# Kernel optimization log

Measured on AMD Instinct MI355X. Metric: run time of the kernel, lower is better.

Reference implementation:

```python
import jax, jax.numpy as jnp
import numpy as np

N, E = 50000, 800000          # nodes, edges
DIN, HEAD, HD = 128, 4, 16    # input dim, heads, per-head dim
DOUT = HEAD * HD              # 64 = head*hd
NEG_SLOPE = 0.01              # torch LeakyReLU default


def _lin(key, fan_in, fan_out):
    # torch nn.Linear default init: U(-1/sqrt(fan_in), 1/sqrt(fan_in))
    kw, kb = jax.random.split(key)
    s = 1.0 / np.sqrt(fan_in)
    W = jax.random.uniform(kw, (fan_in, fan_out), jnp.float32, -s, s)
    b = jax.random.uniform(kb, (fan_out,), jnp.float32, -s, s)
    return W, b


def setup_inputs() -> dict:
    key = jax.random.key(0)
    ks = jax.random.split(key, 8)
    x = jax.random.normal(ks[0], (N, DIN), jnp.float32)
    src = jax.random.randint(ks[1], (E,), 0, N, jnp.int32)
    dst = jax.random.randint(ks[2], (E,), 0, N, jnp.int32)
    Ws, bs = _lin(ks[3], DIN, DOUT)   # relation_aware src linear
    Wd, bd = _lin(ks[4], DIN, DOUT)   # relation_aware dst linear
    Wl, bl = _lin(ks[5], DIN, DOUT)   # w_liner
    Wa, ba = _lin(ks[6], 3 * HD, 1)   # atten
    return dict(x=x, src=src, dst=dst, Ws=Ws, bs=bs, Wd=Wd, bd=bd,
                Wl=Wl, bl=bl, Wa=Wa, ba=ba)


def reference(x, src, dst, Ws, bs, Wd, bd, Wl, bl, Wa, ba):
    # sign_edges: relation-aware per-edge feature edge_sum  [E, DOUT]
    er = jnp.tanh(x[src] @ Ws + bs + (x[dst] @ Wd + bd))

    # w_liner on node features  [N, DOUT]
    h = x @ Wl + bl

    # message: per-edge, per-head concat + linear + leakyrelu score
    sf = h[src].reshape(E, HEAD, HD)
    df = h[dst].reshape(E, HEAD, HD)
    ef = er.reshape(E, HEAD, HD)
    z = jnp.concatenate([sf, df, ef], axis=-1)        # [E, HEAD, 3*HD]
    a = z @ Wa + ba                                    # [E, HEAD, 1]
    a = jnp.where(a >= 0, a, NEG_SLOPE * a)            # leaky relu

    # reduce: mailbox softmax over incoming edges of each dst node
    m = jax.ops.segment_max(a, dst, num_segments=N)    # [N, HEAD, 1]
    m = jnp.where(jnp.isfinite(m), m, 0.0)             # empty mailboxes -> 0
    e = jnp.exp(a - m[dst])
    s = jax.ops.segment_sum(e, dst, num_segments=N)    # [N, HEAD, 1]
    attn = e / jnp.maximum(s[dst], 1e-38)

    out = jax.ops.segment_sum(attn * sf, dst, num_segments=N)
    out = out.reshape(N, DOUT)                         # [N, head*hd]

    # edge_s: mean of edge_sum over incoming edges per node
    deg = jax.ops.segment_sum(jnp.ones((E, 1), x.dtype), dst, num_segments=N)
    edge_s = jax.ops.segment_sum(er, dst, num_segments=N) / jnp.maximum(deg, 1.0)

    return (edge_s, out, h)  # if_sum=False branch: h already [N, head*hd]
```

## Files before the change

kernel.cpp:

```cpp
#include <hip/hip_runtime.h>
#include <math.h>

#define DIN   128
#define DOUT  64
#define NHEAD 4
#define HD    16

typedef __attribute__((ext_vector_type(8))) short bf16x8;
typedef __attribute__((ext_vector_type(8))) unsigned short u16x8;
typedef __attribute__((ext_vector_type(4))) float f32x4;

__device__ __forceinline__ unsigned short f2bf(float f) {
    union { float f; unsigned u; } v; v.f = f;
    unsigned r = v.u + 0x7FFF + ((v.u >> 16) & 1);
    return (unsigned short)(r >> 16);
}
__device__ __forceinline__ float bf2f(unsigned short s) {
    union { unsigned u; float f; } v; v.u = ((unsigned)s) << 16; return v.f;
}

__global__ __launch_bounds__(256)
void k_init(const float* __restrict__ Ws, const float* __restrict__ Wd,
            const float* __restrict__ Wl, short* __restrict__ wT,
            int* __restrict__ degi, int* __restrict__ counter, int N) {
    const int bid = blockIdx.x, tid = threadIdx.x;
    if (bid < 96) {
        const int idx = bid * 256 + tid;
        const int n = idx >> 7, k = idx & 127;
        float v;
        if (n < 64)       v = Ws[k * DOUT + n];
        else if (n < 128) v = Wd[k * DOUT + (n - 64)];
        else              v = Wl[k * DOUT + (n - 128)];
        wT[idx] = (short)f2bf(v);
        if (bid == 0 && tid == 0) *counter = 0;
        return;
    }
    const int i = (bid - 96) * 256 + tid;
    if (i < N) degi[i] = 0;
}

__global__ __launch_bounds__(256)
void k_proj_hist(const float* __restrict__ x, const short* __restrict__ wT,
                 const float* __restrict__ bs, const float* __restrict__ bd,
                 const float* __restrict__ bl, const float* __restrict__ Wa,
                 unsigned short* __restrict__ packed_bf,
                 float* __restrict__ xd, float* __restrict__ alpha_s,
                 float* __restrict__ alpha_d, float* __restrict__ h_out, int N,
                 const int* __restrict__ dst, int* __restrict__ degi,
                 int* __restrict__ rank, int E, int NPJ, int NHB) {
    __shared__ short xs[64 * 136];
    const int bid = blockIdx.x, tid = threadIdx.x;

    if (bid & 1) {
        const int hi = bid >> 1;
        if (hi >= NHB) return;
        const int e0 = (hi * 256 + tid) * 4;
        if (e0 + 3 < E) {
            const int4 d = *(const int4*)&dst[e0];
            int4 r;
            r.x = atomicAdd(&degi[d.x], 1);
            r.y = atomicAdd(&degi[d.y], 1);
            r.z = atomicAdd(&degi[d.z], 1);
            r.w = atomicAdd(&degi[d.w], 1);
            *(int4*)&rank[e0] = r;
        } else {
            for (int e = e0; e < E; ++e) rank[e] = atomicAdd(&degi[dst[e]], 1);
        }
        return;
    }

    const int pj = bid >> 1;
    if (pj >= NPJ) return;
    const int wave = tid >> 6, lane = tid & 63;
    const int lam = lane & 15, g = lane >> 4;
    const int n0 = pj * 64;

    {
        const int r = tid >> 2, c0 = (tid & 3) * 32;
        const int nn = n0 + r;
#pragma unroll
        for (int j = 0; j < 8; ++j) {
            float4 v = make_float4(0.f, 0.f, 0.f, 0.f);
            if (nn < N) v = ((const float4*)x)[(size_t)nn * 32 + (c0 >> 2) + j];
            short4 h4;
            h4.x = (short)f2bf(v.x); h4.y = (short)f2bf(v.y);
            h4.z = (short)f2bf(v.z); h4.w = (short)f2bf(v.w);
            *(short4*)&xs[r * 136 + c0 + j * 4] = h4;
        }
    }
    __syncthreads();

    bf16x8 afr[4];
#pragma unroll
    for (int ks = 0; ks < 4; ++ks)
        afr[ks] = *(const bf16x8*)&xs[(wave * 16 + lam) * 136 + ks * 32 + g * 8];

    f32x4 acc[12];
#pragma unroll
    for (int c = 0; c < 12; ++c) acc[c] = (f32x4){0.f, 0.f, 0.f, 0.f};

#pragma unroll
    for (int c = 0; c < 12; ++c) {
#pragma unroll
        for (int ks = 0; ks < 4; ++ks) {
            const bf16x8 b = *(const bf16x8*)&wT[(c * 16 + lam) * 128 + ks * 32 + g * 8];
            acc[c] = __builtin_amdgcn_mfma_f32_16x16x32_bf16(afr[ks], b, acc[c], 0, 0, 0);
        }
    }

    float bsv[4], bdv[4], blv[4];
#pragma unroll
    for (int c = 0; c < 4; ++c) {
        bsv[c] = bs[c * 16 + lam];
        bdv[c] = bd[c * 16 + lam];
        blv[c] = bl[c * 16 + lam];
    }
    const float waS = Wa[lam], waD = Wa[16 + lam];
    const int cc_base = (lam >> 2), t_sl = lam & 3;

#pragma unroll
    for (int i = 0; i < 4; ++i) {
        const int node = n0 + wave * 16 + g * 4 + i;
        float xsv[4], xdv[4], hv[4];
#pragma unroll
        for (int c = 0; c < 4; ++c) {
            xsv[c] = acc[c][i]     + bsv[c];
            xdv[c] = acc[4 + c][i] + bdv[c];
            hv[c]  = acc[8 + c][i] + blv[c];
        }
        float p0 = hv[0] * waS, p1 = hv[1] * waS, p2 = hv[2] * waS, p3 = hv[3] * waS;
        float q0 = hv[0] * waD, q1 = hv[1] * waD, q2 = hv[2] * waD, q3 = hv[3] * waD;
#pragma unroll
        for (int off = 1; off < 16; off <<= 1) {
            p0 += __shfl_xor(p0, off); p1 += __shfl_xor(p1, off);
            p2 += __shfl_xor(p2, off); p3 += __shfl_xor(p3, off);
            q0 += __shfl_xor(q0, off); q1 += __shfl_xor(q1, off);
            q2 += __shfl_xor(q2, off); q3 += __shfl_xor(q3, off);
        }
        if (node < N) {
            const size_t rowb = (size_t)node * 128;
#pragma unroll
            for (int c = 0; c < 4; ++c) {
                const int cc = c * 4 + cc_base;
                packed_bf[rowb + cc * 8 + t_sl]     = f2bf(xsv[c]);
                packed_bf[rowb + cc * 8 + 4 + t_sl] = f2bf(hv[c]);
                xd   [(size_t)node * DOUT + c * 16 + lam] = xdv[c];
                h_out[(size_t)node * DOUT + c * 16 + lam] = hv[c];
            }
            if (lam == 0) {
                *(f32x4*)&alpha_s[(size_t)node * NHEAD] = (f32x4){p0, p1, p2, p3};
                *(f32x4*)&alpha_d[(size_t)node * NHEAD] = (f32x4){q0, q1, q2, q3};
            }
        }
    }
}

__global__ __launch_bounds__(1024)
void k_scan(const int* __restrict__ degi, int* __restrict__ excl,
            int* __restrict__ bsum, int* __restrict__ boff,
            int* __restrict__ total, int* __restrict__ counter, int N, int NB) {
    __shared__ int wsum[16];
    __shared__ int amLast;
    const int tid = threadIdx.x, lane = tid & 63, wid = tid >> 6;
    const int i = blockIdx.x * 1024 + tid;
    int v = (i < N) ? degi[i] : 0;
    int incl = v;
#pragma unroll
    for (int off = 1; off < 64; off <<= 1) {
        int t = __shfl_up(incl, off);
        if (lane >= off) incl += t;
    }
    if (lane == 63) wsum[wid] = incl;
    __syncthreads();
    if (tid < 16) {
        int t = wsum[tid];
#pragma unroll
        for (int off = 1; off < 16; off <<= 1) {
            int u = __shfl_up(t, off);
            if (tid >= off) t += u;
        }
        wsum[tid] = t;
    }
    __syncthreads();
    const int base = (wid > 0) ? wsum[wid - 1] : 0;
    if (i < N) excl[i] = incl - v + base;
    if (tid == 1023) atomicExch(&bsum[blockIdx.x], wsum[15]);
    __syncthreads();
    if (tid == 0) {
        __threadfence();
        amLast = (atomicAdd(counter, 1) == NB - 1) ? 1 : 0;
    }
    __syncthreads();
    if (amLast && tid < 64) {
        int b = (tid < NB) ? atomicAdd(&bsum[tid], 0) : 0;
        int inc = b;
#pragma unroll
        for (int off = 1; off < 64; off <<= 1) {
            int t = __shfl_up(inc, off);
            if (lane >= off) inc += t;
        }
        if (tid < NB) boff[tid] = inc - b;
        if (tid == 63) *total = inc;
    }
}

__global__ __launch_bounds__(256)
void k_scatter(const int* __restrict__ src, const int* __restrict__ dst,
               const int* __restrict__ rp_raw, const int* __restrict__ boff,
               const int* __restrict__ rank, int* __restrict__ srcs_sorted, int E) {
    const int e0 = (blockIdx.x * 256 + threadIdx.x) * 4;
    if (e0 + 3 < E) {
        const int4 s = *(const int4*)&src[e0];
        const int4 d = *(const int4*)&dst[e0];
        const int4 r = *(const int4*)&rank[e0];
        srcs_sorted[rp_raw[d.x] + boff[d.x >> 10] + r.x] = s.x;
        srcs_sorted[rp_raw[d.y] + boff[d.y >> 10] + r.y] = s.y;
        srcs_sorted[rp_raw[d.z] + boff[d.z >> 10] + r.z] = s.z;
        srcs_sorted[rp_raw[d.w] + boff[d.w >> 10] + r.w] = s.w;
    } else {
        for (int e = e0; e < E; ++e) {
            const int d = dst[e];
            srcs_sorted[rp_raw[d] + boff[d >> 10] + rank[e]] = src[e];
        }
    }
}

__global__ __launch_bounds__(256, 8)
void k_aggregate(const int* __restrict__ rp_raw, const int* __restrict__ boff,
                 const int* __restrict__ total, const int* __restrict__ srcs,
                 const unsigned short* __restrict__ packed_bf,
                 const float* __restrict__ xd,
                 const float* __restrict__ alpha_s, const float* __restrict__ alpha_d,
                 const float* __restrict__ Wa, const float* __restrict__ ba,
                 float* __restrict__ edge_s, float* __restrict__ out, int N) {
    const int lane = threadIdx.x & 63;
    const int n = blockIdx.x * 4 + (threadIdx.x >> 6);
    if (n >= N) return;
    const int g = lane >> 4, lam = lane & 15;
    const int hd = lam >> 2, q = lam & 3;

    const int start = rp_raw[n] + boff[n >> 10];
    const int end = (n + 1 < N) ? (rp_raw[n + 1] + boff[(n + 1) >> 10]) : *total;
    const int deg = end - start;
    const int last = end - 1;

    const float4 xd4 = *(const float4*)&xd[(size_t)n * DOUT + lam * 4];
    const float4 wa4 = *(const float4*)&Wa[32 + q * 4];
    const float adb  = alpha_d[n * NHEAD + hd] + ba[0];

    float es0=0.f,es1=0.f,es2=0.f,es3=0.f;
    float o0=0.f,o1=0.f,o2=0.f,o3=0.f;
    float s = 0.f;

    const int niter = (deg + 3) >> 2;
    int e = start + g;

    float vm0=0.f, vm1=0.f, vm2=0.f;
    u16x8 pk0=(u16x8){0,0,0,0,0,0,0,0}, pk1=pk0, pk2=pk0;
    float as0=0.f, as1=0.f, as2=0.f;
    if (niter > 0) {
        {
            vm0 = (e < end) ? 1.f : 0.f;
            const int sn = srcs[min(e, last)];
            pk0 = *(const u16x8*)&packed_bf[(size_t)sn * 128 + lam * 8];
            as0 = alpha_s[sn * NHEAD + hd];
        }
        {
            const int e1 = e + 4;
            vm1 = (e1 < end) ? 1.f : 0.f;
            const int sn = srcs[min(e1, last)];
            pk1 = *(const u16x8*)&packed_bf[(size_t)sn * 128 + lam * 8];
            as1 = alpha_s[sn * NHEAD + hd];
        }
        {
            const int e2 = e + 8;
            vm2 = (e2 < end) ? 1.f : 0.f;
            const int sn = srcs[min(e2, last)];
            pk2 = *(const u16x8*)&packed_bf[(size_t)sn * 128 + lam * 8];
            as2 = alpha_s[sn * NHEAD + hd];
        }
    }

    for (int it = 0; it < niter; ++it) {
        float vmn = 0.f, asn = 0.f;
        u16x8 pkn = (u16x8){0,0,0,0,0,0,0,0};
        const int e3 = e + 12;
        if (it + 3 < niter) {
            vmn = (e3 < end) ? 1.f : 0.f;
            const int sn = srcs[min(e3, last)];
            pkn = *(const u16x8*)&packed_bf[(size_t)sn * 128 + lam * 8];
            asn = alpha_s[sn * NHEAD + hd];
        }

        const float t0 = __expf(2.f * (bf2f(pk0[0]) + xd4.x));
        const float t1 = __expf(2.f * (bf2f(pk0[1]) + xd4.y));
        const float t2 = __expf(2.f * (bf2f(pk0[2]) + xd4.z));
        const float t3 = __expf(2.f * (bf2f(pk0[3]) + xd4.w));
        const float er0 = fmaf(-2.f, __builtin_amdgcn_rcpf(t0 + 1.f), 1.f);
        const float er1 = fmaf(-2.f, __builtin_amdgcn_rcpf(t1 + 1.f), 1.f);
        const float er2 = fmaf(-2.f, __builtin_amdgcn_rcpf(t2 + 1.f), 1.f);
        const float er3 = fmaf(-2.f, __builtin_amdgcn_rcpf(t3 + 1.f), 1.f);
        es0 = fmaf(er0, vm0, es0); es1 = fmaf(er1, vm0, es1);
        es2 = fmaf(er2, vm0, es2); es3 = fmaf(er3, vm0, es3);

        float p = er0 * wa4.x;
        p = fmaf(er1, wa4.y, p);
        p = fmaf(er2, wa4.z, p);
        p = fmaf(er3, wa4.w, p);
        p += __shfl_xor(p, 1);
        p += __shfl_xor(p, 2);

        float a = as0 + adb + p;
        a = (a >= 0.f) ? a : 0.01f * a;
        const float w = __expf(a) * vm0;
        s += w;
        o0 = fmaf(w, bf2f(pk0[4]), o0); o1 = fmaf(w, bf2f(pk0[5]), o1);
        o2 = fmaf(w, bf2f(pk0[6]), o2); o3 = fmaf(w, bf2f(pk0[7]), o3);

        vm0 = vm1; pk0 = pk1; as0 = as1;
        vm1 = vm2; pk1 = pk2; as1 = as2;
        vm2 = vmn; pk2 = pkn; as2 = asn;
        e += 4;
    }

#pragma unroll
    for (int off = 16; off < 64; off <<= 1) {
        es0 += __shfl_xor(es0, off); es1 += __shfl_xor(es1, off);
        es2 += __shfl_xor(es2, off); es3 += __shfl_xor(es3, off);
        o0  += __shfl_xor(o0,  off); o1  += __shfl_xor(o1,  off);
        o2  += __shfl_xor(o2,  off); o3  += __shfl_xor(o3,  off);
        s   += __shfl_xor(s,   off);
    }

    if (g == 0) {
        const float inv_s = __builtin_amdgcn_rcpf(fmaxf(s, 1e-38f));
        const float inv_d = __builtin_amdgcn_rcpf(fmaxf((float)deg, 1.0f));
        const size_t od = (size_t)n * DOUT + lam * 4;
        *(f32x4*)&out[od]    = (f32x4){o0 * inv_s, o1 * inv_s, o2 * inv_s, o3 * inv_s};
        *(f32x4*)&edge_s[od] = (f32x4){es0 * inv_d, es1 * inv_d, es2 * inv_d, es3 * inv_d};
    }
}

extern "C" void kernel_launch(void* const* d_in, const int* in_sizes, int n_in,
                              void* d_out, int out_size, void* d_ws, size_t ws_size,
                              hipStream_t stream) {
    const float* x  = (const float*)d_in[0];
    const int*   src= (const int*)  d_in[1];
    const int*   dst= (const int*)  d_in[2];
    const float* Ws = (const float*)d_in[3];
    const float* bs = (const float*)d_in[4];
    const float* Wd = (const float*)d_in[5];
    const float* bd = (const float*)d_in[6];
    const float* Wl = (const float*)d_in[7];
    const float* bl = (const float*)d_in[8];
    const float* Wa = (const float*)d_in[9];
    const float* ba = (const float*)d_in[10];

    const int N = in_sizes[0] / DIN;
    const int E = in_sizes[1];
    const int NB = (N + 1023) / 1024;

    float* out_f = (float*)d_out;
    float* edge_s_out = out_f;
    float* out_attn   = out_f + (size_t)N * DOUT;
    float* h_out      = out_f + 2 * (size_t)N * DOUT;

    char* ws = (char*)d_ws;
    size_t o = 0;
    unsigned short* packed_bf = (unsigned short*)(ws + o); o += (size_t)N * 128 * 2;
    float* xd      = (float*)(ws + o); o += (size_t)N * DOUT * 4;
    float* alpha_s = (float*)(ws + o); o += (size_t)N * NHEAD * 4;
    float* alpha_d = (float*)(ws + o); o += (size_t)N * NHEAD * 4;
    int*   degi    = (int*)  (ws + o); o += (size_t)N * 4;
    int*   counter = (int*)  (ws + o); o += 64;
    int*   rp_raw  = (int*)  (ws + o); o += (size_t)(N + 1) * 4;
    int*   rank    = (int*)  (ws + o); o += (size_t)E * 4;
    int*   srcs    = (int*)  (ws + o); o += (size_t)E * 4;
    int*   bsum    = (int*)  (ws + o); o += 64 * 4;
    int*   boff    = (int*)  (ws + o); o += 64 * 4;
    int*   total   = (int*)  (ws + o); o += 64;
    short* wT      = (short*)(ws + o); o += (size_t)192 * 128 * 2;

    k_init<<<96 + (N + 255) / 256, 256, 0, stream>>>(Ws, Wd, Wl, wT, degi, counter, N);

    const int NPJ = (N + 63) / 64;
    const int NHB = (E + 1023) / 1024;
    const int GC  = 2 * ((NPJ > NHB) ? NPJ : NHB);
    k_proj_hist<<<GC, 256, 0, stream>>>(x, wT, bs, bd, bl, Wa,
                                        packed_bf, xd, alpha_s, alpha_d, h_out, N,
                                        dst, degi, rank, E, NPJ, NHB);

    k_scan<<<NB, 1024, 0, stream>>>(degi, rp_raw, bsum, boff, total, counter, N, NB);

    k_scatter<<<((E + 3) / 4 + 255) / 256, 256, 0, stream>>>(src, dst, rp_raw, boff,
                                                             rank, srcs, E);

    k_aggregate<<<(N + 3) / 4, 256, 0, stream>>>(rp_raw, boff, total, srcs,
                                                 packed_bf, xd,
                                                 alpha_s, alpha_d, Wa, ba,
                                                 edge_s_out, out_attn, N);
}
```

Baseline: 130.9 us.

## Replace per-node atomic CSR build with two-level bucket sort by destination

Replaces the per-edge global atomic degree histogram, multi-block scan and scattered rank-based placement with a bucketed counting sort. Edges are first binned into 128-node buckets using shared-memory histograms, then sorted within each bucket in shared memory to produce row_ptr and sorted sources. This removes high-contention global atomics and random scattered writes, at the cost of an extra pass, an intermediate (src,dst) pair buffer and one extra kernel launch. Within-bucket order becomes nondeterministic, so the summation order in aggregation can change.

After: 136.6 us. +4.4%, slower.

```diff
diff --git a/kernel.cpp b/kernel.cpp
--- a/kernel.cpp
+++ b/kernel.cpp
@@ -5,6 +5,8 @@
 #define DOUT  64
 #define NHEAD 4
 #define HD    16
+#define BKT_SH 7
+#define BKT_SZ 128
 
 typedef __attribute__((ext_vector_type(8))) short bf16x8;
 typedef __attribute__((ext_vector_type(8))) unsigned short u16x8;
@@ -22,7 +24,7 @@
 __global__ __launch_bounds__(256)
 void k_init(const float* __restrict__ Ws, const float* __restrict__ Wd,
             const float* __restrict__ Wl, short* __restrict__ wT,
-            int* __restrict__ degi, int* __restrict__ counter, int N) {
+            int* __restrict__ bucket_cnt, int NBK) {
     const int bid = blockIdx.x, tid = threadIdx.x;
     if (bid < 96) {
         const int idx = bid * 256 + tid;
@@ -32,40 +34,47 @@
         else if (n < 128) v = Wd[k * DOUT + (n - 64)];
         else              v = Wl[k * DOUT + (n - 128)];
         wT[idx] = (short)f2bf(v);
-        if (bid == 0 && tid == 0) *counter = 0;
         return;
     }
     const int i = (bid - 96) * 256 + tid;
-    if (i < N) degi[i] = 0;
+    if (i <= NBK) bucket_cnt[i] = 0;
 }
 
 __global__ __launch_bounds__(256)
-void k_proj_hist(const float* __restrict__ x, const short* __restrict__ wT,
-                 const float* __restrict__ bs, const float* __restrict__ bd,
-                 const float* __restrict__ bl, const float* __restrict__ Wa,
-                 unsigned short* __restrict__ packed_bf,
-                 float* __restrict__ xd, float* __restrict__ alpha_s,
-                 float* __restrict__ alpha_d, float* __restrict__ h_out, int N,
-                 const int* __restrict__ dst, int* __restrict__ degi,
-                 int* __restrict__ rank, int E, int NPJ, int NHB) {
+void k_proj_cnt(const float* __restrict__ x, const short* __restrict__ wT,
+                const float* __restrict__ bs, const float* __restrict__ bd,
+                const float* __restrict__ bl, const float* __restrict__ Wa,
+                unsigned short* __restrict__ packed_bf,
+                float* __restrict__ xd, float* __restrict__ alpha_s,
+                float* __restrict__ alpha_d, float* __restrict__ h_out, int N,
+                const int* __restrict__ dst, int* __restrict__ bucket_cnt,
+                int E, int NPJ, int NCB, int NBK) {
     __shared__ short xs[64 * 136];
+    __shared__ int  lhist[392];
     const int bid = blockIdx.x, tid = threadIdx.x;
 
     if (bid & 1) {
-        const int hi = bid >> 1;
-        if (hi >= NHB) return;
-        const int e0 = (hi * 256 + tid) * 4;
-        if (e0 + 3 < E) {
-            const int4 d = *(const int4*)&dst[e0];
-            int4 r;
-            r.x = atomicAdd(&degi[d.x], 1);
-            r.y = atomicAdd(&degi[d.y], 1);
-            r.z = atomicAdd(&degi[d.z], 1);
-            r.w = atomicAdd(&degi[d.w], 1);
-            *(int4*)&rank[e0] = r;
-        } else {
-            for (int e = e0; e < E; ++e) rank[e] = atomicAdd(&degi[dst[e]], 1);
-        }
+        const int ci = bid >> 1;
+        if (ci >= NCB) return;
+        for (int i = tid; i < NBK; i += 256) lhist[i] = 0;
+        __syncthreads();
+        const int base0 = ci * 4096;
+#pragma unroll
+        for (int k = 0; k < 4; ++k) {
+            const int e0 = base0 + k * 1024 + tid * 4;
+            if (e0 + 3 < E) {
+                const int4 d = *(const int4*)&dst[e0];
+                atomicAdd(&lhist[d.x >> BKT_SH], 1);
+                atomicAdd(&lhist[d.y >> BKT_SH], 1);
+                atomicAdd(&lhist[d.z >> BKT_SH], 1);
+                atomicAdd(&lhist[d.w >> BKT_SH], 1);
+            } else {
+                for (int e = e0; e < E; ++e) atomicAdd(&lhist[dst[e] >> BKT_SH], 1);
+            }
+        }
+        __syncthreads();
+        for (int i = tid; i < NBK; i += 256)
+            if (lhist[i]) atomicAdd(&bucket_cnt[i], lhist[i]);
         return;
     }
 
@@ -155,15 +164,13 @@
     }
 }
 
-__global__ __launch_bounds__(1024)
-void k_scan(const int* __restrict__ degi, int* __restrict__ excl,
-            int* __restrict__ bsum, int* __restrict__ boff,
-            int* __restrict__ total, int* __restrict__ counter, int N, int NB) {
-    __shared__ int wsum[16];
-    __shared__ int amLast;
+__global__ __launch_bounds__(512)
+void k_scan_buckets(const int* __restrict__ bucket_cnt,
+                    int* __restrict__ bucket_base, int* __restrict__ bucket_cursor,
+                    int NBK) {
+    __shared__ int wsum[8];
     const int tid = threadIdx.x, lane = tid & 63, wid = tid >> 6;
-    const int i = blockIdx.x * 1024 + tid;
-    int v = (i < N) ? degi[i] : 0;
+    int v = (tid < NBK) ? bucket_cnt[tid] : 0;
     int incl = v;
 #pragma unroll
     for (int off = 1; off < 64; off <<= 1) {
@@ -172,10 +179,10 @@
     }
     if (lane == 63) wsum[wid] = incl;
     __syncthreads();
-    if (tid < 16) {
+    if (tid < 8) {
         int t = wsum[tid];
 #pragma unroll
-        for (int off = 1; off < 16; off <<= 1) {
+        for (int off = 1; off < 8; off <<= 1) {
             int u = __shfl_up(t, off);
             if (tid >= off) t += u;
         }
@@ -183,51 +190,110 @@
     }
     __syncthreads();
     const int base = (wid > 0) ? wsum[wid - 1] : 0;
-    if (i < N) excl[i] = incl - v + base;
-    if (tid == 1023) atomicExch(&bsum[blockIdx.x], wsum[15]);
-    __syncthreads();
-    if (tid == 0) {
-        __threadfence();
-        amLast = (atomicAdd(counter, 1) == NB - 1) ? 1 : 0;
-    }
-    __syncthreads();
-    if (amLast && tid < 64) {
-        int b = (tid < NB) ? atomicAdd(&bsum[tid], 0) : 0;
-        int inc = b;
+    const int excl = incl - v + base;
+    if (tid < NBK) {
+        bucket_base[tid]   = excl;
+        bucket_cursor[tid] = excl;
+    }
+    if (tid == 0) bucket_base[NBK] = wsum[7];
+}
+
+__global__ __launch_bounds__(256)
+void k_bucket_scatter(const int* __restrict__ src, const int* __restrict__ dst,
+                      int* __restrict__ bucket_cursor, int2* __restrict__ pairs,
+                      int E, int NBK) {
+    __shared__ int lhist[392];
+    __shared__ int lcur[392];
+    const int tid = threadIdx.x;
+    const int base0 = blockIdx.x * 4096;
+    for (int i = tid; i < NBK; i += 256) lhist[i] = 0;
+    __syncthreads();
+#pragma unroll
+    for (int k = 0; k < 4; ++k) {
+        const int e0 = base0 + k * 1024 + tid * 4;
+        if (e0 + 3 < E) {
+            const int4 d = *(const int4*)&dst[e0];
+            atomicAdd(&lhist[d.x >> BKT_SH], 1);
+            atomicAdd(&lhist[d.y >> BKT_SH], 1);
+            atomicAdd(&lhist[d.z >> BKT_SH], 1);
+            atomicAdd(&lhist[d.w >> BKT_SH], 1);
+        } else {
+            for (int e = e0; e < E; ++e) atomicAdd(&lhist[dst[e] >> BKT_SH], 1);
+        }
+    }
+    __syncthreads();
+    for (int i = tid; i < NBK; i += 256)
+        lcur[i] = lhist[i] ? atomicAdd(&bucket_cursor[i], lhist[i]) : 0;
+    __syncthreads();
+#pragma unroll
+    for (int k = 0; k < 4; ++k) {
+        const int e0 = base0 + k * 1024 + tid * 4;
+        if (e0 + 3 < E) {
+            const int4 s = *(const int4*)&src[e0];
+            const int4 d = *(const int4*)&dst[e0];
+            int p;
+            p = atomicAdd(&lcur[d.x >> BKT_SH], 1); pairs[p] = make_int2(s.x, d.x);
+            p = atomicAdd(&lcur[d.y >> BKT_SH], 1); pairs[p] = make_int2(s.y, d.y);
+            p = atomicAdd(&lcur[d.z >> BKT_SH], 1); pairs[p] = make_int2(s.z, d.z);
+            p = atomicAdd(&lcur[d.w >> BKT_SH], 1); pairs[p] = make_int2(s.w, d.w);
+        } else {
+            for (int e = e0; e < E; ++e) {
+                const int d = dst[e];
+                const int p = atomicAdd(&lcur[d >> BKT_SH], 1);
+                pairs[p] = make_int2(src[e], d);
+            }
+        }
+    }
+}
+
+__global__ __launch_bounds__(256)
+void k_bucket_rank(const int2* __restrict__ pairs, const int* __restrict__ bucket_base,
+                   int* __restrict__ row_ptr, int* __restrict__ srcs,
+                   int N, int NBK) {
+    __shared__ int hist[BKT_SZ];
+    __shared__ int cursor[BKT_SZ];
+    __shared__ int wtot[2];
+    const int b = blockIdx.x, tid = threadIdx.x;
+    const int n0 = b << BKT_SH;
+    const int ebase = bucket_base[b];
+    const int ecnt  = bucket_base[b + 1] - ebase;
+
+    if (tid < BKT_SZ) hist[tid] = 0;
+    __syncthreads();
+    for (int i = tid; i < ecnt; i += 256)
+        atomicAdd(&hist[pairs[ebase + i].y & (BKT_SZ - 1)], 1);
+    __syncthreads();
+
+    int v = 0, incl = 0;
+    const int lane = tid & 63, wid = tid >> 6;
+    if (tid < BKT_SZ) {
+        v = hist[tid];
+        incl = v;
 #pragma unroll
         for (int off = 1; off < 64; off <<= 1) {
-            int t = __shfl_up(inc, off);
-            if (lane >= off) inc += t;
-        }
-        if (tid < NB) boff[tid] = inc - b;
-        if (tid == 63) *total = inc;
-    }
-}
-
-__global__ __launch_bounds__(256)
-void k_scatter(const int* __restrict__ src, const int* __restrict__ dst,
-               const int* __restrict__ rp_raw, const int* __restrict__ boff,
-               const int* __restrict__ rank, int* __restrict__ srcs_sorted, int E) {
-    const int e0 = (blockIdx.x * 256 + threadIdx.x) * 4;
-    if (e0 + 3 < E) {
-        const int4 s = *(const int4*)&src[e0];
-        const int4 d = *(const int4*)&dst[e0];
-        const int4 r = *(const int4*)&rank[e0];
-        srcs_sorted[rp_raw[d.x] + boff[d.x >> 10] + r.x] = s.x;
-        srcs_sorted[rp_raw[d.y] + boff[d.y >> 10] + r.y] = s.y;
-        srcs_sorted[rp_raw[d.z] + boff[d.z >> 10] + r.z] = s.z;
-        srcs_sorted[rp_raw[d.w] + boff[d.w >> 10] + r.w] = s.w;
-    } else {
-        for (int e = e0; e < E; ++e) {
-            const int d = dst[e];
-            srcs_sorted[rp_raw[d] + boff[d >> 10] + rank[e]] = src[e];
-        }
+            int t = __shfl_up(incl, off);
+            if (lane >= off) incl += t;
+        }
+        if (lane == 63) wtot[wid] = incl;
+    }
+    __syncthreads();
+    if (tid < BKT_SZ) {
+        const int excl = incl - v + ((wid == 1) ? wtot[0] : 0);
+        if (n0 + tid < N) row_ptr[n0 + tid] = ebase + excl;
+        cursor[tid] = excl;
+    }
+    if (b == NBK - 1 && tid == 0) row_ptr[N] = bucket_base[NBK];
+    __syncthreads();
+
+    for (int i = tid; i < ecnt; i += 256) {
+        const int2 pr = pairs[ebase + i];
+        const int slot = atomicAdd(&cursor[pr.y & (BKT_SZ - 1)], 1);
+        srcs[ebase + slot] = pr.x;
     }
 }
 
 __global__ __launch_bounds__(256, 8)
-void k_aggregate(const int* __restrict__ rp_raw, const int* __restrict__ boff,
-                 const int* __restrict__ total, const int* __restrict__ srcs,
+void k_aggregate(const int* __restrict__ row_ptr, const int* __restrict__ srcs,
                  const unsigned short* __restrict__ packed_bf,
                  const float* __restrict__ xd,
                  const float* __restrict__ alpha_s, const float* __restrict__ alpha_d,
@@ -239,8 +305,8 @@
     const int g = lane >> 4, lam = lane & 15;
     const int hd = lam >> 2, q = lam & 3;
 
-    const int start = rp_raw[n] + boff[n >> 10];
-    const int end = (n + 1 < N) ? (rp_raw[n + 1] + boff[(n + 1) >> 10]) : *total;
+    const int start = row_ptr[n];
+    const int end   = row_ptr[n + 1];
     const int deg = end - start;
     const int last = end - 1;
 
@@ -358,7 +424,7 @@
 
     const int N = in_sizes[0] / DIN;
     const int E = in_sizes[1];
-    const int NB = (N + 1023) / 1024;
+    const int NBK = (N + BKT_SZ - 1) >> BKT_SH;
 
     float* out_f = (float*)d_out;
     float* edge_s_out = out_f;
@@ -371,32 +437,30 @@
     float* xd      = (float*)(ws + o); o += (size_t)N * DOUT * 4;
     float* alpha_s = (float*)(ws + o); o += (size_t)N * NHEAD * 4;
     float* alpha_d = (float*)(ws + o); o += (size_t)N * NHEAD * 4;
-    int*   degi    = (int*)  (ws + o); o += (size_t)N * 4;
-    int*   counter = (int*)  (ws + o); o += 64;
-    int*   rp_raw  = (int*)  (ws + o); o += (size_t)(N + 1) * 4;
-    int*   rank    = (int*)  (ws + o); o += (size_t)E * 4;
+    int*   row_ptr = (int*)  (ws + o); o += (size_t)(N + 1) * 4;
     int*   srcs    = (int*)  (ws + o); o += (size_t)E * 4;
-    int*   bsum    = (int*)  (ws + o); o += 64 * 4;
-    int*   boff    = (int*)  (ws + o); o += 64 * 4;
-    int*   total   = (int*)  (ws + o); o += 64;
+    int2*  pairs   = (int2*) (ws + o); o += (size_t)E * 8;
+    int*   bucket_cnt    = (int*)(ws + o); o += 512 * 4;
+    int*   bucket_base   = (int*)(ws + o); o += 513 * 4;
+    int*   bucket_cursor = (int*)(ws + o); o += 512 * 4;
     short* wT      = (short*)(ws + o); o += (size_t)192 * 128 * 2;
 
-    k_init<<<96 + (N + 255) / 256, 256, 0, stream>>>(Ws, Wd, Wl, wT, degi, counter, N);
+    k_init<<<96 + (NBK + 256) / 256, 256, 0, stream>>>(Ws, Wd, Wl, wT, bucket_cnt, NBK);
 
     const int NPJ = (N + 63) / 64;
-    const int NHB = (E + 1023) / 1024;
-    const int GC  = 2 * ((NPJ > NHB) ? NPJ : NHB);
-    k_proj_hist<<<GC, 256, 0, stream>>>(x, wT, bs, bd, bl, Wa,
-                                        packed_bf, xd, alpha_s, alpha_d, h_out, N,
-                                        dst, degi, rank, E, NPJ, NHB);
-
-    k_scan<<<NB, 1024, 0, stream>>>(degi, rp_raw, bsum, boff, total, counter, N, NB);
-
-    k_scatter<<<((E + 3) / 4 + 255) / 256, 256, 0, stream>>>(src, dst, rp_raw, boff,
-                                                             rank, srcs, E);
-
-    k_aggregate<<<(N + 3) / 4, 256, 0, stream>>>(rp_raw, boff, total, srcs,
-                                                 packed_bf, xd,
+    const int NCB = (E + 4095) / 4096;
+    const int GC  = 2 * ((NPJ > NCB) ? NPJ : NCB);
+    k_proj_cnt<<<GC, 256, 0, stream>>>(x, wT, bs, bd, bl, Wa,
+                                       packed_bf, xd, alpha_s, alpha_d, h_out, N,
+                                       dst, bucket_cnt, E, NPJ, NCB, NBK);
+
+    k_scan_buckets<<<1, 512, 0, stream>>>(bucket_cnt, bucket_base, bucket_cursor, NBK);
+
+    k_bucket_scatter<<<NCB, 256, 0, stream>>>(src, dst, bucket_cursor, pairs, E, NBK);
+
+    k_bucket_rank<<<NBK, 256, 0, stream>>>(pairs, bucket_base, row_ptr, srcs, N, NBK);
+
+    k_aggregate<<<(N + 3) / 4, 256, 0, stream>>>(row_ptr, srcs, packed_bf, xd,
                                                  alpha_s, alpha_d, Wa, ba,
                                                  edge_s_out, out_attn, N);
 }
```
